# Kernel optimization log

Measured on AMD Instinct MI355X. Metric: run time of the kernel, lower is better.

## Reference

```python
import jax, jax.numpy as jnp
import numpy as np

INP_DIM, OUT_DIM, MID_DIM, MID_LAYERS = 3, 1, 4, 2


def _uniform(key, shape, bound):
    return jax.random.uniform(key, shape, jnp.float32, -bound, bound)


def setup_inputs() -> dict:
    key = jax.random.key(0)
    ks = jax.random.split(key, 16)
    B, T = 4096, 1024
    bnd = 1.0 / np.sqrt(MID_DIM)  # PyTorch LSTM/Linear init bound
    d = {
        "x": jax.random.normal(ks[0], (B, T, INP_DIM), jnp.float32),
        # layer 0 LSTM (gate order i,f,g,o stacked along rows)
        "W_ih0": _uniform(ks[1], (4 * MID_DIM, INP_DIM), bnd),
        "W_hh0": _uniform(ks[2], (4 * MID_DIM, MID_DIM), bnd),
        "b_ih0": _uniform(ks[3], (4 * MID_DIM,), bnd),
        "b_hh0": _uniform(ks[4], (4 * MID_DIM,), bnd),
        # layer 1 LSTM
        "W_ih1": _uniform(ks[5], (4 * MID_DIM, MID_DIM), bnd),
        "W_hh1": _uniform(ks[6], (4 * MID_DIM, MID_DIM), bnd),
        "b_ih1": _uniform(ks[7], (4 * MID_DIM,), bnd),
        "b_hh1": _uniform(ks[8], (4 * MID_DIM,), bnd),
        "W1": _uniform(ks[9], (MID_DIM, MID_DIM), bnd),
        "b1": _uniform(ks[10], (MID_DIM,), bnd),
        "W2": _uniform(ks[11], (OUT_DIM, MID_DIM), bnd),
        "b2": _uniform(ks[12], (OUT_DIM,), bnd),
    }
    return d


def _lstm_layer(x_tbd, W_ih, W_hh, b_ih, b_hh):
    # x_tbd: [T, B, D] time-major. Precompute input contribution to all gates.
    H = W_hh.shape[1]
    xg = jnp.einsum("tbd,gd->tbg", x_tbd, W_ih) + (b_ih + b_hh)  # [T,B,4H]

    def step(carry, xg_t):
        h, c = carry
        g = xg_t + h @ W_hh.T  # [B,4H]
        i, f, gg, o = jnp.split(g, 4, axis=-1)
        i = jax.nn.sigmoid(i)
        f = jax.nn.sigmoid(f)
        gg = jnp.tanh(gg)
        o = jax.nn.sigmoid(o)
        c = f * c + i * gg
        h = o * jnp.tanh(c)
        return (h, c), h

    B = x_tbd.shape[1]
    init = (jnp.zeros((B, H), x_tbd.dtype), jnp.zeros((B, H), x_tbd.dtype))
    _, hs = jax.lax.scan(step, init, xg)
    return hs  # [T,B,H]


def reference(x, W_ih0, W_hh0, b_ih0, b_hh0, W_ih1, W_hh1, b_ih1, b_hh1, W1, b1, W2, b2):
    # x: [B,T,3] (batch_first). Run 2-layer LSTM then per-timestep MLP head.
    h = jnp.transpose(x, (1, 0, 2))  # -> [T,B,3]
    h = _lstm_layer(h, W_ih0, W_hh0, b_ih0, b_hh0)
    h = _lstm_layer(h, W_ih1, W_hh1, b_ih1, b_hh1)
    h = jnp.transpose(h, (1, 0, 2))  # -> [B,T,H]
    y = jnp.tanh(h @ W1.T + b1) @ W2.T + b2  # [B,T,1]
    return y
```

## Files before the change

### kernel.cpp

```cpp
#include <hip/hip_runtime.h>


#define T_STEPS 1024
#define BATCH   4096
#define CHUNK   16
#define NCHUNK  (T_STEPS / CHUNK)
#define RDEPTH  4

__device__ __forceinline__ float fast_exp2(float x) {
#if __has_builtin(__builtin_amdgcn_exp2f)
    return __builtin_amdgcn_exp2f(x);
#else
    return exp2f(x);
#endif
}

__device__ __forceinline__ float fast_rcp(float x) {
#if __has_builtin(__builtin_amdgcn_rcpf)
    return __builtin_amdgcn_rcpf(x);
#else
    return 1.0f / x;
#endif
}

__device__ __forceinline__ float fast_tanh(float x) {
    return 2.0f * fast_rcp(1.0f + fast_exp2(-2.88539008f * x)) - 1.0f;
}

template <int CTRL>
__device__ __forceinline__ float dpp_mov(float v) {
    int i = __builtin_bit_cast(int, v);
    i = __builtin_amdgcn_mov_dpp(i, CTRL, 0xF, 0xF, true);
    return __builtin_bit_cast(float, i);
}

#define DPP_QB0         0x00
#define DPP_QB1         0x55
#define DPP_QB2         0xAA
#define DPP_QB3         0xFF
#define DPP_ROR8        0x128
#define DPP_MIRROR      0x140
#define DPP_HALF_MIRROR 0x141
#define DPP_QSWAP2      0x4E
#define DPP_QSWAP1      0xB1

__global__ __launch_bounds__(768) void lstm_r11_kernel(
    const float* __restrict__ x,
    const float* __restrict__ W_ih0, const float* __restrict__ W_hh0,
    const float* __restrict__ b_ih0, const float* __restrict__ b_hh0,
    const float* __restrict__ W_ih1, const float* __restrict__ W_hh1,
    const float* __restrict__ b_ih1, const float* __restrict__ b_hh1,
    const float* __restrict__ W1, const float* __restrict__ b1,
    const float* __restrict__ W2, const float* __restrict__ b2,
    float* __restrict__ out)
{
    __shared__ float4 xstage[4][2][68];
    __shared__ float4 ring0[4][RDEPTH][CHUNK][4];
    __shared__ float4 ring1[4][RDEPTH][CHUNK][4];
    __shared__ int done0[4][RDEPTH];
    __shared__ int free0[4][RDEPTH];
    __shared__ int done1[4][RDEPTH];
    __shared__ int free1[4][RDEPTH];

    const int tid  = threadIdx.x;
    const int wave = tid >> 6;
    const int stg  = wave >> 2;
    const int pr   = wave & 3;
    const int lane = tid & 63;
    const int idx  = lane & 15;
    const int rho  = lane & 3;
    const int u    = (lane >> 2) & 3;
    const int r    = rho * 4 + u;
    const int ch   = lane >> 4;
    const int batch = blockIdx.x * 16 + pr * 4 + ch;

    if (tid < 4 * RDEPTH) {
        done0[tid >> 2][tid & 3] = 0;
        free0[tid >> 2][tid & 3] = 0;
        done1[tid >> 2][tid & 3] = 0;
        free1[tid >> 2][tid & 3] = 0;
    }
    __syncthreads();

    const float am = (rho == 2) ? -2.88539008f : -1.44269504f;
    const float aa = (rho == 2) ? 2.0f : 1.0f;
    const float ab = (rho == 2) ? -1.0f : 0.0f;

    if (stg == 0) {
        const float wx0 = W_ih0[r * 3 + 0];
        const float wx1 = W_ih0[r * 3 + 1];
        const float wx2 = W_ih0[r * 3 + 2];
        const float bias0 = b_ih0[r] + b_hh0[r];
        float wh0[4];
#pragma unroll
        for (int k = 0; k < 4; ++k) wh0[k] = W_hh0[r * 4 + (u ^ k)];

        float h0 = 0.f, c0 = 0.f, h0b = 0.f, h0c = 0.f, h0d = 0.f;

        const float* xrow = x + (size_t)batch * T_STEPS * 3;
        const float* p0 = xrow + idx * 3;
        xstage[pr][0][ch * 17 + idx] = make_float4(p0[0], p0[1], p0[2], 0.f);
        const float* p1 = xrow + 48 + idx * 3;
        float q0 = p1[0], q1 = p1[1], q2 = p1[2];

        volatile int* ff = &free0[pr][0];

        for (int c = 0; c < NCHUNK; ++c) {
            const int s = c & (RDEPTH - 1);
            if (c >= RDEPTH) {
                while (ff[s] < c - RDEPTH + 1) { __builtin_amdgcn_s_sleep(1); }
            }

            const float4* xs = &xstage[pr][c & 1][ch * 17];
            float xg[CHUNK];
#pragma unroll
            for (int tt = 0; tt < CHUNK; ++tt) {
                float4 xv = xs[tt];
                xg[tt] = bias0 + wx0 * xv.x + wx1 * xv.y + wx2 * xv.z;
            }

            float hs0[CHUNK];
#pragma unroll
            for (int tt = 0; tt < CHUNK; ++tt) {
                float pre0 = xg[tt]
                           + wh0[0] * h0 + wh0[1] * h0b + wh0[2] * h0c + wh0[3] * h0d;
                float a0 = aa * fast_rcp(1.0f + fast_exp2(am * pre0)) + ab;
                float gi = dpp_mov<DPP_QB0>(a0);
                float gf = dpp_mov<DPP_QB1>(a0);
                float gg = dpp_mov<DPP_QB2>(a0);
                float go = dpp_mov<DPP_QB3>(a0);
                c0 = gf * c0 + gi * gg;
                h0 = go * fast_tanh(c0);
                h0b = dpp_mov<DPP_HALF_MIRROR>(h0);
                h0c = dpp_mov<DPP_ROR8>(h0);
                h0d = dpp_mov<DPP_MIRROR>(h0);
                hs0[tt] = h0;
            }

            if (rho == 0) {
                float* rw = &((float*)&ring0[pr][s][0][ch])[u];
#pragma unroll
                for (int tt = 0; tt < CHUNK; ++tt) rw[tt * 16] = hs0[tt];
            }
            __threadfence_block();
            if (lane == 0) done0[pr][s] = c + 1;

            if (c < NCHUNK - 1)
                xstage[pr][(c + 1) & 1][ch * 17 + idx] = make_float4(q0, q1, q2, 0.f);
            if (c < NCHUNK - 2) {
                const float* p = xrow + (c + 2) * 48 + idx * 3;
                q0 = p[0]; q1 = p[1]; q2 = p[2];
            }
        }
    } else if (stg == 1) {
        const float bias1 = b_ih1[r] + b_hh1[r];
        float wi1[4], wh1[4];
#pragma unroll
        for (int k = 0; k < 4; ++k) {
            wi1[k] = W_ih1[r * 4 + k];
            wh1[k] = W_hh1[r * 4 + (u ^ k)];
        }

        float h1 = 0.f, c1 = 0.f, h1b = 0.f, h1c = 0.f, h1d = 0.f;

        volatile int* df = &done0[pr][0];
        volatile int* f1 = &free1[pr][0];

        for (int c = 0; c < NCHUNK; ++c) {
            const int s = c & (RDEPTH - 1);
            while (df[s] < c + 1) { __builtin_amdgcn_s_sleep(1); }
            if (c >= RDEPTH) {
                while (f1[s] < c - RDEPTH + 1) { __builtin_amdgcn_s_sleep(1); }
            }
            __threadfence_block();

            const float4* rgp = &ring0[pr][s][0][ch];
            float xb[CHUNK];
#pragma unroll
            for (int tt = 0; tt < CHUNK; ++tt) {
                float4 hv = rgp[tt * 4];
                xb[tt] = bias1 + wi1[0] * hv.x + wi1[1] * hv.y
                               + wi1[2] * hv.z + wi1[3] * hv.w;
            }

            float hs1[CHUNK];
#pragma unroll
            for (int tt = 0; tt < CHUNK; ++tt) {
                float pre1 = xb[tt]
                           + wh1[0] * h1 + wh1[1] * h1b + wh1[2] * h1c + wh1[3] * h1d;
                float a1 = aa * fast_rcp(1.0f + fast_exp2(am * pre1)) + ab;
                float gi1 = dpp_mov<DPP_QB0>(a1);
                float gf1 = dpp_mov<DPP_QB1>(a1);
                float gg1 = dpp_mov<DPP_QB2>(a1);
                float go1 = dpp_mov<DPP_QB3>(a1);
                c1 = gf1 * c1 + gi1 * gg1;
                h1 = go1 * fast_tanh(c1);
                h1b = dpp_mov<DPP_HALF_MIRROR>(h1);
                h1c = dpp_mov<DPP_ROR8>(h1);
                h1d = dpp_mov<DPP_MIRROR>(h1);
                hs1[tt] = h1;
            }

            if (rho == 0) {
                float* rw = &((float*)&ring1[pr][s][0][ch])[u];
#pragma unroll
                for (int tt = 0; tt < CHUNK; ++tt) rw[tt * 16] = hs1[tt];
            }
            if (lane == 0) free0[pr][s] = c + 1;
            __threadfence_block();
            if (lane == 0) done1[pr][s] = c + 1;
        }
    } else {
        const int cu  = lane & 3;
        const int sb  = (lane >> 2) & 3;
        const int cch = lane >> 4;
        const int cbatch = blockIdx.x * 16 + pr * 4 + cch;

        float w1r[4];
#pragma unroll
        for (int k = 0; k < 4; ++k) w1r[k] = W1[cu * 4 + k];
        const float b1u = b1[cu];
        const float w2u = W2[cu];
        const float b2v = b2[0];
        float* op = out + (size_t)cbatch * T_STEPS;

        volatile int* d1 = &done1[pr][0];

        for (int c = 0; c < NCHUNK; ++c) {
            const int s = c & (RDEPTH - 1);
            while (d1[s] < c + 1) { __builtin_amdgcn_s_sleep(1); }
            __threadfence_block();

            const float4* rg = &ring1[pr][s][sb][cch];
            float yq[4];
#pragma unroll
            for (int it = 0; it < 4; ++it) {
                float4 h = rg[it * 16];
                float zp = b1u + w1r[0] * h.x + w1r[1] * h.y
                               + w1r[2] * h.z + w1r[3] * h.w;
                float z  = fast_tanh(zp);
                float yv = w2u * z;
                float t1 = yv + dpp_mov<DPP_QSWAP2>(yv);
                yq[it]   = t1 + dpp_mov<DPP_QSWAP1>(t1) + b2v;
            }
            if (lane == 0) free1[pr][s] = c + 1;

            if (cu == 0) {
#pragma unroll
                for (int it = 0; it < 4; ++it)
                    op[c * CHUNK + it * 4 + sb] = yq[it];
            }
        }
    }
}

extern "C" void kernel_launch(void* const* d_in, const int* in_sizes, int n_in,
                              void* d_out, int out_size, void* d_ws, size_t ws_size,
                              hipStream_t stream) {
    const float* x     = (const float*)d_in[0];
    const float* W_ih0 = (const float*)d_in[1];
    const float* W_hh0 = (const float*)d_in[2];
    const float* b_ih0 = (const float*)d_in[3];
    const float* b_hh0 = (const float*)d_in[4];
    const float* W_ih1 = (const float*)d_in[5];
    const float* W_hh1 = (const float*)d_in[6];
    const float* b_ih1 = (const float*)d_in[7];
    const float* b_hh1 = (const float*)d_in[8];
    const float* W1    = (const float*)d_in[9];
    const float* b1    = (const float*)d_in[10];
    const float* W2    = (const float*)d_in[11];
    const float* b2    = (const float*)d_in[12];
    float* out = (float*)d_out;

    dim3 grid(BATCH / 16);
    dim3 block(768);
    lstm_r11_kernel<<<grid, block, 0, stream>>>(
        x, W_ih0, W_hh0, b_ih0, b_hh0, W_ih1, W_hh1, b_ih1, b_hh1,
        W1, b1, W2, b2, out);
}
```

Before: 229.9 us.

## Software-pipeline LSTM stage input projections and add wave priorities

New measurement: 244.6 us. +6.4%, slower.

```diff
diff --git a/kernel.cpp b/kernel.cpp
--- a/kernel.cpp
+++ b/kernel.cpp
@@ -44,7 +44,7 @@
 #define DPP_QSWAP2      0x4E
 #define DPP_QSWAP1      0xB1
 
-__global__ __launch_bounds__(768) void lstm_r11_kernel(
+__global__ __launch_bounds__(768) void lstm_r12_kernel(
     const float* __restrict__ x,
     const float* __restrict__ W_ih0, const float* __restrict__ W_hh0,
     const float* __restrict__ b_ih0, const float* __restrict__ b_hh0,
@@ -87,6 +87,7 @@
     const float ab = (rho == 2) ? -1.0f : 0.0f;
 
     if (stg == 0) {
+        __builtin_amdgcn_s_setprio(1);
         const float wx0 = W_ih0[r * 3 + 0];
         const float wx1 = W_ih0[r * 3 + 1];
         const float wx2 = W_ih0[r * 3 + 2];
@@ -103,26 +104,31 @@
         const float* p1 = xrow + 48 + idx * 3;
         float q0 = p1[0], q1 = p1[1], q2 = p1[2];
 
-        volatile int* ff = &free0[pr][0];
-
-        for (int c = 0; c < NCHUNK; ++c) {
-            const int s = c & (RDEPTH - 1);
-            if (c >= RDEPTH) {
-                while (ff[s] < c - RDEPTH + 1) { __builtin_amdgcn_s_sleep(1); }
-            }
-
-            const float4* xs = &xstage[pr][c & 1][ch * 17];
-            float xg[CHUNK];
+        float xgA[CHUNK], xgB[CHUNK];
+        {
+            const float4* xs = &xstage[pr][0][ch * 17];
 #pragma unroll
             for (int tt = 0; tt < CHUNK; ++tt) {
                 float4 xv = xs[tt];
-                xg[tt] = bias0 + wx0 * xv.x + wx1 * xv.y + wx2 * xv.z;
+                xgA[tt] = bias0 + wx0 * xv.x + wx1 * xv.y + wx2 * xv.z;
+            }
+        }
+
+        volatile int* ff = &free0[pr][0];
+
+        auto a_chunk = [&](int c, float (&xg_cur)[CHUNK], float (&xg_nxt)[CHUNK]) {
+            const int s = c & (RDEPTH - 1);
+            if (c < NCHUNK - 1)
+                xstage[pr][(c + 1) & 1][ch * 17 + idx] = make_float4(q0, q1, q2, 0.f);
+            if (c < NCHUNK - 2) {
+                const float* p = xrow + (c + 2) * 48 + idx * 3;
+                q0 = p[0]; q1 = p[1]; q2 = p[2];
             }
 
             float hs0[CHUNK];
 #pragma unroll
             for (int tt = 0; tt < CHUNK; ++tt) {
-                float pre0 = xg[tt]
+                float pre0 = xg_cur[tt]
                            + wh0[0] * h0 + wh0[1] * h0b + wh0[2] * h0c + wh0[3] * h0d;
                 float a0 = aa * fast_rcp(1.0f + fast_exp2(am * pre0)) + ab;
                 float gi = dpp_mov<DPP_QB0>(a0);
@@ -137,6 +143,18 @@
                 hs0[tt] = h0;
             }
 
+            if (c < NCHUNK - 1) {
+                const float4* xs = &xstage[pr][(c + 1) & 1][ch * 17];
+#pragma unroll
+                for (int tt = 0; tt < CHUNK; ++tt) {
+                    float4 xv = xs[tt];
+                    xg_nxt[tt] = bias0 + wx0 * xv.x + wx1 * xv.y + wx2 * xv.z;
+                }
+            }
+
+            if (c >= RDEPTH) {
+                while (ff[s] < c - RDEPTH + 1) { __builtin_amdgcn_s_sleep(1); }
+            }
             if (rho == 0) {
                 float* rw = &((float*)&ring0[pr][s][0][ch])[u];
 #pragma unroll
@@ -144,15 +162,14 @@
             }
             __threadfence_block();
             if (lane == 0) done0[pr][s] = c + 1;
-
-            if (c < NCHUNK - 1)
-                xstage[pr][(c + 1) & 1][ch * 17 + idx] = make_float4(q0, q1, q2, 0.f);
-            if (c < NCHUNK - 2) {
-                const float* p = xrow + (c + 2) * 48 + idx * 3;
-                q0 = p[0]; q1 = p[1]; q2 = p[2];
-            }
+        };
+
+        for (int c = 0; c < NCHUNK; c += 2) {
+            a_chunk(c, xgA, xgB);
+            a_chunk(c + 1, xgB, xgA);
         }
     } else if (stg == 1) {
+        __builtin_amdgcn_s_setprio(2);
         const float bias1 = b_ih1[r] + b_hh1[r];
         float wi1[4], wh1[4];
 #pragma unroll
@@ -166,27 +183,32 @@
         volatile int* df = &done0[pr][0];
         volatile int* f1 = &free1[pr][0];
 
-        for (int c = 0; c < NCHUNK; ++c) {
-            const int s = c & (RDEPTH - 1);
-            while (df[s] < c + 1) { __builtin_amdgcn_s_sleep(1); }
-            if (c >= RDEPTH) {
-                while (f1[s] < c - RDEPTH + 1) { __builtin_amdgcn_s_sleep(1); }
-            }
-            __threadfence_block();
-
-            const float4* rgp = &ring0[pr][s][0][ch];
-            float xb[CHUNK];
+        float xbA[CHUNK], xbB[CHUNK];
+        while (df[0] < 1) { __builtin_amdgcn_s_sleep(1); }
+        __threadfence_block();
+        {
+            const float4* rgp = &ring0[pr][0][0][ch];
 #pragma unroll
             for (int tt = 0; tt < CHUNK; ++tt) {
                 float4 hv = rgp[tt * 4];
-                xb[tt] = bias1 + wi1[0] * hv.x + wi1[1] * hv.y
-                               + wi1[2] * hv.z + wi1[3] * hv.w;
+                xbA[tt] = bias1 + wi1[0] * hv.x + wi1[1] * hv.y
+                                + wi1[2] * hv.z + wi1[3] * hv.w;
+            }
+        }
+
+        auto b_chunk = [&](int c, float (&xb_cur)[CHUNK], float (&xb_nxt)[CHUNK]) {
+            const int s = c & (RDEPTH - 1);
+            if (lane == 0) free0[pr][s] = c + 1;
+
+            if (c < NCHUNK - 1) {
+                while (df[(c + 1) & (RDEPTH - 1)] < c + 2) { __builtin_amdgcn_s_sleep(1); }
+                __threadfence_block();
             }
 
             float hs1[CHUNK];
 #pragma unroll
             for (int tt = 0; tt < CHUNK; ++tt) {
-                float pre1 = xb[tt]
+                float pre1 = xb_cur[tt]
                            + wh1[0] * h1 + wh1[1] * h1b + wh1[2] * h1c + wh1[3] * h1d;
                 float a1 = aa * fast_rcp(1.0f + fast_exp2(am * pre1)) + ab;
                 float gi1 = dpp_mov<DPP_QB0>(a1);
@@ -201,14 +223,31 @@
                 hs1[tt] = h1;
             }
 
+            if (c < NCHUNK - 1) {
+                const float4* rgp = &ring0[pr][(c + 1) & (RDEPTH - 1)][0][ch];
+#pragma unroll
+                for (int tt = 0; tt < CHUNK; ++tt) {
+                    float4 hv = rgp[tt * 4];
+                    xb_nxt[tt] = bias1 + wi1[0] * hv.x + wi1[1] * hv.y
+                                       + wi1[2] * hv.z + wi1[3] * hv.w;
+                }
+            }
+
+            if (c >= RDEPTH) {
+                while (f1[s] < c - RDEPTH + 1) { __builtin_amdgcn_s_sleep(1); }
+            }
             if (rho == 0) {
                 float* rw = &((float*)&ring1[pr][s][0][ch])[u];
 #pragma unroll
                 for (int tt = 0; tt < CHUNK; ++tt) rw[tt * 16] = hs1[tt];
             }
-            if (lane == 0) free0[pr][s] = c + 1;
             __threadfence_block();
             if (lane == 0) done1[pr][s] = c + 1;
+        };
+
+        for (int c = 0; c < NCHUNK; c += 2) {
+            b_chunk(c, xbA, xbB);
+            b_chunk(c + 1, xbB, xbA);
         }
     } else {
         const int cu  = lane & 3;
@@ -274,7 +313,7 @@
 
     dim3 grid(BATCH / 16);
     dim3 block(768);
-    lstm_r11_kernel<<<grid, block, 0, stream>>>(
+    lstm_r12_kernel<<<grid, block, 0, stream>>>(
         x, W_ih0, W_hh0, b_ih0, b_hh0, W_ih1, W_hh1, b_ih1, b_hh1,
         W1, b1, W2, b2, out);
 }
```
